# Kernel tuning notes

Hardware: AMD Instinct MI355X
Metric: run time of the kernel (lower is better)

## Reference

```python
import jax, jax.numpy as jnp
import numpy as np

D_MODEL = 1024
D_FF = 4096
FFN_H = int(2 * D_FF / 3)  # 2730, per SwiGLUMLP
B, S = 4, 4096
LN_EPS = 1e-5
ATTN_EPS = 1e-6


def layer_norm(x, g, b):
    mu = jnp.mean(x, axis=-1, keepdims=True)
    var = jnp.mean(jnp.square(x - mu), axis=-1, keepdims=True)
    return (x - mu) * jax.lax.rsqrt(var + LN_EPS) * g + b


def setup_inputs() -> dict:
    key = jax.random.key(0)
    ks = jax.random.split(key, 16)
    s = 0.02
    return {
        "x": jax.random.normal(ks[0], (B, S, D_MODEL), dtype=jnp.float32),
        "Wqkv": jax.random.normal(ks[1], (D_MODEL, 3 * D_MODEL), dtype=jnp.float32) * s,
        "bqkv": jnp.zeros((3 * D_MODEL,), jnp.float32),
        "Wg": jax.random.normal(ks[2], (D_MODEL, FFN_H), dtype=jnp.float32) * s,
        "bg": jnp.zeros((FFN_H,), jnp.float32),
        "Wu": jax.random.normal(ks[3], (D_MODEL, FFN_H), dtype=jnp.float32) * s,
        "bu": jnp.zeros((FFN_H,), jnp.float32),
        "Wd": jax.random.normal(ks[4], (FFN_H, D_MODEL), dtype=jnp.float32) * s,
        "bd": jnp.zeros((D_MODEL,), jnp.float32),
        "g1": jnp.ones((D_MODEL,), jnp.float32),
        "b1": jnp.zeros((D_MODEL,), jnp.float32),
        "g2": jnp.ones((D_MODEL,), jnp.float32),
        "b2": jnp.zeros((D_MODEL,), jnp.float32),
    }


def reference(x, Wqkv, bqkv, Wg, bg, Wu, bu, Wd, bd, g1, b1, g2, b2):
    # QKV projection, split into q, k, v (each [B,S,D])
    qkv = jnp.einsum("bsd,de->bse", x, Wqkv) + bqkv
    q, k, v = jnp.split(qkv, 3, axis=-1)

    # Linear attention with elu(x)+1 feature map (non-causal)
    qp = jax.nn.elu(q) + 1.0
    kp = jax.nn.elu(k) + 1.0
    kv = jnp.einsum("bsd,bse->bde", kp, v)        # [B,D,D] context
    num = jnp.einsum("bsd,bde->bse", qp, kv)       # [B,S,D]
    k_sum = jnp.sum(kp, axis=1)                    # [B,D]
    den = jnp.einsum("bsd,bd->bs", qp, k_sum)[..., None]
    attn = num / (den + ATTN_EPS)

    x = layer_norm(x + attn, g1, b1)

    # SwiGLU MLP
    gate = jnp.einsum("bsd,dh->bsh", x, Wg) + bg
    up = jnp.einsum("bsd,dh->bsh", x, Wu) + bu
    ffn = jnp.einsum("bsh,hd->bsd", jax.nn.silu(gate) * up, Wd) + bd

    return layer_norm(x + ffn, g2, b2)
```

## Files before the change

### kernel.cpp

```cpp
#include <hip/hip_runtime.h>

#define SEQ 4096
#define TOK 16384
#define DM 1024
#define NQKV 3072
#define FFH 2730
#define FFHP 2816

typedef __bf16 bf16x8 __attribute__((ext_vector_type(8)));
typedef float f32x4 __attribute__((ext_vector_type(4)));

__device__ __forceinline__ unsigned short f2bf(float f) {
  union { float f; unsigned u; } v; v.f = f;
  unsigned r = v.u + 0x7fffu + ((v.u >> 16) & 1u);
  return (unsigned short)(r >> 16);
}
__device__ __forceinline__ float bf2f(unsigned short h) {
  union { unsigned u; float f; } v; v.u = ((unsigned)h) << 16;
  return v.f;
}

__device__ __forceinline__ void xcd_swizzle(int& bx, int& by) {
  const int gx = gridDim.x, gy = gridDim.y;
  const int chunk = gy >> 3;
  const int csh = __ffs(chunk) - 1;
  const int lin = by * gx + bx;
  const int xcd = lin & 7, j = lin >> 3;
  by = xcd * chunk + (j & (chunk - 1));
  bx = j >> csh;
}

enum { M_QKV = 0, M_BF16 = 1, M_NUM = 2, M_BIAS_F32 = 5 };

template<int MODE>
__global__ __launch_bounds__(256)
void gemm_kernel(const unsigned short* __restrict__ A,
                 const unsigned short* __restrict__ BT,
                 int K, int lda, int ldb, int ldc,
                 long zsA, long zsB, long zsC,
                 void* __restrict__ out0, void* __restrict__ out1, void* __restrict__ out2,
                 const float* __restrict__ bias, int nbias)
{
  __shared__ unsigned short As[2][128 * 64];
  __shared__ unsigned short Bs[2][128 * 64];
  const int tid  = threadIdx.x;
  const int wave = tid >> 6, lane = tid & 63;
  const int quad = lane >> 4, l16 = lane & 15;
  const int bz = blockIdx.z;
  int bx = blockIdx.x, by = blockIdx.y;
  xcd_swizzle(bx, by);

  const unsigned short* Ab = A + (size_t)zsA * bz + (size_t)by * 128 * lda;
  const unsigned short* Bb = BT + (size_t)zsB * bz + (size_t)bx * 128 * ldb;

  f32x4 acc[4][4] = {};

  const int srow   = lane >> 3;
  const int scol_g = (((lane & 7) ^ srow) * 8);
  const int axor   = l16 & 7;

  auto stage = [&](int buf, int k0) {
#pragma unroll
    for (int j = 0; j < 4; ++j) {
      int c = wave * 4 + j;
      const unsigned short* sa = Ab + (size_t)(c * 8 + srow) * lda + k0 + scol_g;
      __builtin_amdgcn_global_load_lds((__attribute__((address_space(1))) void*)sa,
          (__attribute__((address_space(3))) void*)(As[buf] + c * 512), 16, 0, 0);
      const unsigned short* sb = Bb + (size_t)(c * 8 + srow) * ldb + k0 + scol_g;
      __builtin_amdgcn_global_load_lds((__attribute__((address_space(1))) void*)sb,
          (__attribute__((address_space(3))) void*)(Bs[buf] + c * 512), 16, 0, 0);
    }
  };

  const int NIT = K >> 6;
  stage(0, 0);
  int cur = 0;
  for (int it = 0; it < NIT; ++it) {
    __builtin_amdgcn_s_waitcnt(0);
    __syncthreads();
    if (it + 1 < NIT) stage(cur ^ 1, (it + 1) << 6);
#pragma unroll
    for (int kk = 0; kk < 64; kk += 32) {
      bf16x8 af[4], bfr[4];
#pragma unroll
      for (int mt = 0; mt < 4; ++mt)
        af[mt] = *(const bf16x8*)(As[cur] + ((wave >> 1) * 64 + mt * 16 + l16) * 64
                                     + ((((kk >> 3) + quad) ^ axor) * 8));
#pragma unroll
      for (int nt = 0; nt < 4; ++nt)
        bfr[nt] = *(const bf16x8*)(Bs[cur] + ((wave & 1) * 64 + nt * 16 + l16) * 64
                                      + ((((kk >> 3) + quad) ^ axor) * 8));
#pragma unroll
      for (int mt = 0; mt < 4; ++mt)
#pragma unroll
        for (int nt = 0; nt < 4; ++nt)
          acc[mt][nt] = __builtin_amdgcn_mfma_f32_16x16x32_bf16(af[mt], bfr[nt], acc[mt][nt], 0, 0, 0);
    }
    cur ^= 1;
  }

#pragma unroll
  for (int mt = 0; mt < 4; ++mt) {
#pragma unroll
    for (int nt = 0; nt < 4; ++nt) {
      const int r0 = by * 128 + (wave >> 1) * 64 + mt * 16 + quad * 4;
      const int c  = bx * 128 + (wave & 1) * 64 + nt * 16 + l16;
      float vals[4];
#pragma unroll
      for (int i = 0; i < 4; ++i) vals[i] = acc[mt][nt][i];

      if (MODE == M_QKV) {
        const int b = r0 >> 12, s0 = r0 & 4095;
#pragma unroll
        for (int i = 0; i < 4; ++i) vals[i] += bias[c];
        if (c < 1024) {
#pragma unroll
          for (int i = 0; i < 4; ++i) {
            float e = vals[i] > 0.f ? vals[i] + 1.f : __expf(vals[i]);
            ((unsigned short*)out0)[(size_t)(r0 + i) * DM + c] = f2bf(e);
          }
        } else if (c < 2048) {
          ushort4 o;
          float e0 = vals[0] > 0.f ? vals[0] + 1.f : __expf(vals[0]);
          float e1 = vals[1] > 0.f ? vals[1] + 1.f : __expf(vals[1]);
          float e2 = vals[2] > 0.f ? vals[2] + 1.f : __expf(vals[2]);
          float e3 = vals[3] > 0.f ? vals[3] + 1.f : __expf(vals[3]);
          o.x = f2bf(e0); o.y = f2bf(e1); o.z = f2bf(e2); o.w = f2bf(e3);
          *(ushort4*)((unsigned short*)out1 + (size_t)b * DM * SEQ + (size_t)(c - 1024) * SEQ + s0) = o;
        } else {
          ushort4 o;
          o.x = f2bf(vals[0]); o.y = f2bf(vals[1]); o.z = f2bf(vals[2]); o.w = f2bf(vals[3]);
          *(ushort4*)((unsigned short*)out2 + (size_t)b * DM * SEQ + (size_t)(c - 2048) * SEQ + s0) = o;
        }
      } else {
#pragma unroll
        for (int i = 0; i < 4; ++i) {
          const int r = r0 + i;
          float val = vals[i];
          if (MODE == M_BF16 || MODE == M_NUM) {
            ((unsigned short*)out0)[(size_t)zsC * bz + (size_t)r * ldc + c] = f2bf(val);
          } else {
            if (c < nbias) val += bias[c];
            ((float*)out0)[(size_t)r * ldc + c] = val;
          }
        }
      }
    }
  }
}

enum { G_GATEUP = 0, G_NUM = 1, G_BIAS_F32 = 2 };

#define MBAR() asm volatile("s_barrier" ::: "memory")
#define WAITV(N) asm volatile("s_waitcnt vmcnt(" #N ")" ::: "memory")

#define LDS_A(BUF, QM) do {                                                   \
    _Pragma("unroll")                                                         \
    for (int mt = 0; mt < 4; ++mt) {                                          \
      _Pragma("unroll")                                                       \
      for (int k2 = 0; k2 < 2; ++k2)                                          \
        af[mt][k2] = *(const bf16x8*)(As[BUF] +                               \
            (wm * 128 + ((QM) * 4 + mt) * 16 + l16) * 64 +                    \
            (((k2 * 4 + quad) ^ axor) * 8));                                  \
    }                                                                         \
  } while (0)

#define LDS_B(BUF, QN) do {                                                   \
    _Pragma("unroll")                                                         \
    for (int nt = 0; nt < 2; ++nt) {                                          \
      _Pragma("unroll")                                                       \
      for (int k2 = 0; k2 < 2; ++k2)                                          \
        bfr[nt][k2] = *(const bf16x8*)(Bs[BUF] +                              \
            (wn * 64 + ((QN) * 2 + nt) * 16 + l16) * 64 +                     \
            (((k2 * 4 + quad) ^ axor) * 8));                                  \
    }                                                                         \
  } while (0)

#define MMAQ(QM, QN) do {                                                     \
    _Pragma("unroll")                                                         \
    for (int mt = 0; mt < 4; ++mt) {                                          \
      _Pragma("unroll")                                                       \
      for (int nt = 0; nt < 2; ++nt) {                                        \
        _Pragma("unroll")                                                     \
        for (int k2 = 0; k2 < 2; ++k2)                                        \
          acc[(QM) * 4 + mt][(QN) * 2 + nt] =                                 \
              __builtin_amdgcn_mfma_f32_16x16x32_bf16(af[mt][k2], bfr[nt][k2],\
                  acc[(QM) * 4 + mt][(QN) * 2 + nt], 0, 0, 0);                \
      }                                                                       \
    }                                                                         \
  } while (0)

#define PHASE(BUF, QM, QN, LA, LB, STAGE, WAIT) do {                          \
    if (LA) LDS_A(BUF, QM);                                                   \
    if (LB) LDS_B(BUF, QN);                                                   \
    STAGE                                                                     \
    MBAR();                                                                   \
    __builtin_amdgcn_sched_barrier(0);                                        \
    __builtin_amdgcn_s_setprio(1);                                            \
    MMAQ(QM, QN);                                                             \
    __builtin_amdgcn_s_setprio(0);                                            \
    WAIT                                                                      \
    MBAR();                                                                   \
  } while (0)

template<int MODE>
__global__ __launch_bounds__(512, 2)
void gemm256_kernel(const unsigned short* __restrict__ A,
                    const unsigned short* __restrict__ BT,
                    int K, int lda, int ldb, int ldc,
                    long zsA, long zsB, long zsC,
                    void* __restrict__ out0,
                    const float* __restrict__ bias0,
                    const float* __restrict__ bias1,
                    int nbias)
{
  __shared__ unsigned short As[2][256 * 64];
  __shared__ unsigned short Bs[2][256 * 64];
  const int tid  = threadIdx.x;
  const int wave = tid >> 6, lane = tid & 63;
  const int quad = lane >> 4, l16 = lane & 15;
  const int wm = wave >> 2, wn = wave & 3;
  const int bz = blockIdx.z;
  int bx = blockIdx.x, by = blockIdx.y;
  xcd_swizzle(bx, by);

  const unsigned short* Ab = A + (size_t)zsA * bz + (size_t)by * 256 * lda;
  const unsigned short* Bb = BT + (size_t)zsB * bz + (size_t)bx * 256 * ldb;

  f32x4 acc[8][4] = {};

  const int srow = lane >> 3;
  const int sxor = ((lane & 7) ^ srow) * 8;
  const int axor = l16 & 7;

  const unsigned short* pA[2][2];
  const unsigned short* pB[2][2];
  int cA[2][2], cB[2][2];
#pragma unroll
  for (int part = 0; part < 2; ++part) {
#pragma unroll
    for (int j = 0; j < 2; ++j) {
      int idx = wave * 2 + j;
      int ca = ((idx & 8) ? idx + 8 : idx) + part * 8;
      int cb = (idx >> 2) * 8 + (idx & 3) + part * 4;
      cA[part][j] = ca; cB[part][j] = cb;
      pA[part][j] = Ab + (size_t)(ca * 8 + srow) * lda + sxor;
      pB[part][j] = Bb + (size_t)(cb * 8 + srow) * ldb + sxor;
    }
  }

  auto stageA = [&](int buf, int part, int tile) {
    const int k0 = tile << 6;
#pragma unroll
    for (int j = 0; j < 2; ++j)
      __builtin_amdgcn_global_load_lds(
          (__attribute__((address_space(1))) void*)(pA[part][j] + k0),
          (__attribute__((address_space(3))) void*)(As[buf] + cA[part][j] * 512), 16, 0, 0);
  };
  auto stageB = [&](int buf, int part, int tile) {
    const int k0 = tile << 6;
#pragma unroll
    for (int j = 0; j < 2; ++j)
      __builtin_amdgcn_global_load_lds(
          (__attribute__((address_space(1))) void*)(pB[part][j] + k0),
          (__attribute__((address_space(3))) void*)(Bs[buf] + cB[part][j] * 512), 16, 0, 0);
  };

  stageA(0, 0, 0); stageA(0, 1, 0); stageB(0, 0, 0); stageB(0, 1, 0);
  stageB(1, 0, 1); stageA(1, 1, 1);
  WAITV(4);
  MBAR();

  bf16x8 af[4][2], bfr[2][2];
  const int NT = K >> 6;
  for (int i = 0; i < NT; i += 2) {
    const int t1 = i + 1;
    const int t2s = (i + 2 < NT), t3s = (i + 3 < NT);
    PHASE(0, 0, 0, 1, 1, { stageA(1, 0, t1); }, {});
    PHASE(0, 1, 0, 1, 0, { stageB(1, 1, t1); }, {});
    PHASE(0, 1, 1, 0, 1, { if (t2s) stageB(0, 0, i + 2); }, {});
    PHASE(0, 0, 1, 1, 0, { if (t2s) stageA(0, 1, i + 2); },
                         { if (t2s) { WAITV(4); } else { WAITV(0); } });
    PHASE(1, 0, 0, 1, 1, { if (t2s) stageA(0, 0, i + 2); }, {});
    PHASE(1, 1, 0, 1, 0, { if (t2s) stageB(0, 1, i + 2); }, {});
    PHASE(1, 1, 1, 0, 1, { if (t3s) stageB(1, 0, i + 3); }, {});
    PHASE(1, 0, 1, 1, 0, { if (t3s) stageA(1, 1, i + 3); },
                         { if (t3s) { WAITV(4); } else { WAITV(0); } });
  }

  if (MODE == G_GATEUP) {
#pragma unroll
    for (int mt = 0; mt < 8; ++mt) {
      const int r0 = by * 256 + wm * 128 + mt * 16 + quad * 4;
#pragma unroll
      for (int p = 0; p < 2; ++p) {
        const int hc = bx * 128 + wn * 32 + p * 16 + l16;
        const float bgv = (hc < nbias) ? bias0[hc] : 0.f;
        const float buv = (hc < nbias) ? bias1[hc] : 0.f;
#pragma unroll
        for (int i2 = 0; i2 < 4; ++i2) {
          float g = acc[mt][2 * p][i2] + bgv;
          float u = acc[mt][2 * p + 1][i2] + buv;
          float hv = g / (1.f + __expf(-g)) * u;
          ((unsigned short*)out0)[(size_t)(r0 + i2) * ldc + hc] = f2bf(hv);
        }
      }
    }
  } else {
#pragma unroll
    for (int mt = 0; mt < 8; ++mt) {
#pragma unroll
      for (int nt = 0; nt < 4; ++nt) {
        const int r0 = by * 256 + wm * 128 + mt * 16 + quad * 4;
        const int c  = bx * 256 + wn * 64 + nt * 16 + l16;
#pragma unroll
        for (int i2 = 0; i2 < 4; ++i2) {
          float v = acc[mt][nt][i2];
          if (MODE == G_NUM) {
            ((unsigned short*)out0)[(size_t)zsC * bz + (size_t)(r0 + i2) * ldc + c] = f2bf(v);
          } else {
            if (c < nbias) v += bias0[c];
            ((float*)out0)[(size_t)(r0 + i2) * ldc + c] = v;
          }
        }
      }
    }
  }
}

__global__ __launch_bounds__(256)
void cvt_kernel(const float* __restrict__ in, unsigned short* __restrict__ out, int n)
{
  int i = (blockIdx.x * 256 + threadIdx.x) * 4;
  if (i < n) {
    float4 v = *(const float4*)(in + i);
    ushort4 o;
    o.x = f2bf(v.x); o.y = f2bf(v.y); o.z = f2bf(v.z); o.w = f2bf(v.w);
    *(ushort4*)(out + i) = o;
  }
}

__global__ __launch_bounds__(256)
void wtrans_kernel(const float* __restrict__ in, unsigned short* __restrict__ out,
                   int R, int C, int Cpad, int Rpad, int omode)
{
  __shared__ float tile[32][33];
  int r0 = blockIdx.x * 32;
  int c0 = blockIdx.y * 32;
  int tid = threadIdx.x;
#pragma unroll
  for (int j = 0; j < 4; ++j) {
    int r = j * 8 + (tid >> 5), c = tid & 31;
    float v = 0.f;
    if (r0 + r < R && c0 + c < C) v = in[(size_t)(r0 + r) * C + c0 + c];
    tile[r][c] = v;
  }
  __syncthreads();
#pragma unroll
  for (int j = 0; j < 4; ++j) {
    int c = j * 8 + (tid >> 5), r = tid & 31;
    int oc = c0 + c;
    int orow = (omode == 0) ? oc
             : ((oc >> 4) * 32 + (oc & 15) + ((omode == 2) ? 16 : 0));
    out[(size_t)orow * Rpad + (r0 + r)] = f2bf(tile[r][c]);
  }
}

__device__ __forceinline__ float block_sum(float v, float* sm)
{
#pragma unroll
  for (int o = 32; o > 0; o >>= 1) v += __shfl_down(v, o, 64);
  int w = threadIdx.x >> 6;
  if ((threadIdx.x & 63) == 0) sm[w] = v;
  __syncthreads();
  float r = sm[0] + sm[1] + sm[2] + sm[3];
  __syncthreads();
  return r;
}

__global__ __launch_bounds__(256)
void ksum_kernel(const unsigned short* __restrict__ kpT, float* __restrict__ ksum)
{
  __shared__ float sm[4];
  int row = blockIdx.x;
  const ushort4* src = (const ushort4*)(kpT + (size_t)row * SEQ);
  float s = 0.f;
#pragma unroll
  for (int j = 0; j < 4; ++j) {
    ushort4 v = src[threadIdx.x + j * 256];
    s += bf2f(v.x) + bf2f(v.y) + bf2f(v.z) + bf2f(v.w);
  }
  float tot = block_sum(s, sm);
  if (threadIdx.x == 0) ksum[row] = tot;
}

__global__ __launch_bounds__(256)
void ln1_kernel(const unsigned short* __restrict__ xb16, const unsigned short* __restrict__ num16,
                const unsigned short* __restrict__ qp, const float* __restrict__ ksum,
                const float* __restrict__ g1, const float* __restrict__ b1,
                unsigned short* __restrict__ yb)
{
  __shared__ float sm[4];
  int t = blockIdx.x, tid = threadIdx.x, b = t >> 12;
  ushort4 xv = ((const ushort4*)(xb16 + (size_t)t * DM))[tid];
  ushort4 nv = ((const ushort4*)(num16 + (size_t)t * DM))[tid];
  ushort4 qv = ((const ushort4*)(qp + (size_t)t * DM))[tid];
  float4 kv = ((const float4*)(ksum + (size_t)b * DM))[tid];
  float q0 = bf2f(qv.x), q1 = bf2f(qv.y), q2 = bf2f(qv.z), q3 = bf2f(qv.w);
  float den = block_sum(q0 * kv.x + q1 * kv.y + q2 * kv.z + q3 * kv.w, sm);
  float inv = 1.f / (den + 1e-6f);
  float r0 = bf2f(xv.x) + bf2f(nv.x) * inv, r1 = bf2f(xv.y) + bf2f(nv.y) * inv;
  float r2 = bf2f(xv.z) + bf2f(nv.z) * inv, r3 = bf2f(xv.w) + bf2f(nv.w) * inv;
  float s1 = block_sum(r0 + r1 + r2 + r3, sm);
  float s2 = block_sum(r0 * r0 + r1 * r1 + r2 * r2 + r3 * r3, sm);
  float mu = s1 * (1.f / 1024.f);
  float var = s2 * (1.f / 1024.f) - mu * mu;
  float rs = rsqrtf(var + 1e-5f);
  float4 gv = ((const float4*)g1)[tid];
  float4 bv = ((const float4*)b1)[tid];
  ushort4 o;
  o.x = f2bf((r0 - mu) * rs * gv.x + bv.x);
  o.y = f2bf((r1 - mu) * rs * gv.y + bv.y);
  o.z = f2bf((r2 - mu) * rs * gv.z + bv.z);
  o.w = f2bf((r3 - mu) * rs * gv.w + bv.w);
  ((ushort4*)(yb + (size_t)t * DM))[tid] = o;
}

__global__ __launch_bounds__(256)
void ln2_kernel(const unsigned short* __restrict__ yb, const float* __restrict__ ffn,
                const float* __restrict__ g2, const float* __restrict__ b2,
                float* __restrict__ out)
{
  __shared__ float sm[4];
  int t = blockIdx.x, tid = threadIdx.x;
  ushort4 yv = ((const ushort4*)(yb + (size_t)t * DM))[tid];
  float4 fv = ((const float4*)(ffn + (size_t)t * DM))[tid];
  float r0 = bf2f(yv.x) + fv.x, r1 = bf2f(yv.y) + fv.y;
  float r2 = bf2f(yv.z) + fv.z, r3 = bf2f(yv.w) + fv.w;
  float s1 = block_sum(r0 + r1 + r2 + r3, sm);
  float s2 = block_sum(r0 * r0 + r1 * r1 + r2 * r2 + r3 * r3, sm);
  float mu = s1 * (1.f / 1024.f);
  float var = s2 * (1.f / 1024.f) - mu * mu;
  float rs = rsqrtf(var + 1e-5f);
  float4 gv = ((const float4*)g2)[tid];
  float4 bv = ((const float4*)b2)[tid];
  float4 o;
  o.x = (r0 - mu) * rs * gv.x + bv.x;
  o.y = (r1 - mu) * rs * gv.y + bv.y;
  o.z = (r2 - mu) * rs * gv.z + bv.z;
  o.w = (r3 - mu) * rs * gv.w + bv.w;
  ((float4*)(out + (size_t)t * DM))[tid] = o;
}

extern "C" void kernel_launch(void* const* d_in, const int* in_sizes, int n_in,
                              void* d_out, int out_size, void* d_ws, size_t ws_size,
                              hipStream_t stream)
{
  const float* x    = (const float*)d_in[0];
  const float* Wqkv = (const float*)d_in[1];
  const float* bqkv = (const float*)d_in[2];
  const float* Wg   = (const float*)d_in[3];
  const float* bg   = (const float*)d_in[4];
  const float* Wu   = (const float*)d_in[5];
  const float* bu   = (const float*)d_in[6];
  const float* Wd   = (const float*)d_in[7];
  const float* bd   = (const float*)d_in[8];
  const float* g1   = (const float*)d_in[9];
  const float* b1   = (const float*)d_in[10];
  const float* g2   = (const float*)d_in[11];
  const float* b2   = (const float*)d_in[12];
  float* out = (float*)d_out;

  char* ws = (char*)d_ws;
  size_t off = 0;
  auto alloc = [&](size_t bytes) {
    char* p = ws + off;
    off += (bytes + 255) & ~(size_t)255;
    return p;
  };
  unsigned short* WqkvT = (unsigned short*)alloc((size_t)NQKV * DM * 2);
  unsigned short* WguT  = (unsigned short*)alloc((size_t)2 * FFHP * DM * 2);
  unsigned short* WdT   = (unsigned short*)alloc((size_t)DM * FFHP * 2);
  float*          ksum  = (float*)alloc((size_t)4 * DM * 4);
  unsigned short* xbyb  = (unsigned short*)alloc((size_t)TOK * DM * 2);
  unsigned short* kvT   = (unsigned short*)alloc((size_t)4 * DM * DM * 2);
  char* R3 = alloc((size_t)3 * TOK * DM * 2);
  unsigned short* qp  = (unsigned short*)(R3);
  unsigned short* kpT = (unsigned short*)(R3 + (size_t)TOK * DM * 2);
  unsigned short* vT  = (unsigned short*)(R3 + (size_t)2 * TOK * DM * 2);
  unsigned short* hbuf = (unsigned short*)(R3);
  unsigned short* xb = xbyb;
  unsigned short* yb = xbyb;
  unsigned short* num = (unsigned short*)d_out;
  float* ffn = (float*)d_out;

  dim3 blk(256), blk5(512);

  cvt_kernel<<<dim3(TOK * DM / 1024), blk, 0, stream>>>(x, xb, TOK * DM);
  wtrans_kernel<<<dim3(32, 96), blk, 0, stream>>>(Wqkv, WqkvT, 1024, 3072, 3072, 1024, 0);
  wtrans_kernel<<<dim3(32, 88), blk, 0, stream>>>(Wg, WguT, 1024, FFH, FFHP, 1024, 1);
  wtrans_kernel<<<dim3(32, 88), blk, 0, stream>>>(Wu, WguT, 1024, FFH, FFHP, 1024, 2);
  wtrans_kernel<<<dim3(88, 32), blk, 0, stream>>>(Wd, WdT, FFH, 1024, 1024, FFHP, 0);
  gemm_kernel<M_QKV><<<dim3(NQKV / 128, TOK / 128), blk, 0, stream>>>(
      xb, WqkvT, 1024, 1024, 1024, 0, 0, 0, 0, qp, kpT, vT, bqkv, NQKV);
  ksum_kernel<<<dim3(4096), blk, 0, stream>>>(kpT, ksum);
  gemm_kernel<M_BF16><<<dim3(8, 8, 4), blk, 0, stream>>>(
      vT, kpT, 4096, 4096, 4096, 1024,
      (long)DM * SEQ, (long)DM * SEQ, (long)DM * DM,
      kvT, nullptr, nullptr, nullptr, 0);
  gemm256_kernel<G_NUM><<<dim3(4, 16, 4), blk5, 0, stream>>>(
      qp, kvT, 1024, 1024, 1024, 1024,
      (long)SEQ * DM, (long)DM * DM, (long)SEQ * DM,
      num, nullptr, nullptr, 0);
  ln1_kernel<<<dim3(TOK), blk, 0, stream>>>(xb, num, qp, ksum, g1, b1, yb);
  gemm256_kernel<G_GATEUP><<<dim3(2 * FFHP / 256, TOK / 256), blk5, 0, stream>>>(
      yb, WguT, 1024, DM, DM, FFHP, 0, 0, 0, hbuf, bg, bu, FFH);
  gemm256_kernel<G_BIAS_F32><<<dim3(DM / 256, TOK / 256), blk5, 0, stream>>>(
      hbuf, WdT, FFHP, FFHP, FFHP, DM, 0, 0, 0, ffn, bd, nullptr, DM);
  ln2_kernel<<<dim3(TOK), blk, 0, stream>>>(yb, ffn, g2, b2, out);

  (void)in_sizes; (void)n_in; (void)out_size; (void)ws_size;
}
```

Before: 787.7 us.

## Move QKV projection onto 256x256 pipelined GEMM with LDS-transposed K/V epilogue

New measurement: 741.2 us. -5.9%, faster.

```diff
diff --git a/kernel.cpp b/kernel.cpp
--- a/kernel.cpp
+++ b/kernel.cpp
@@ -9,6 +9,7 @@
 
 typedef __bf16 bf16x8 __attribute__((ext_vector_type(8)));
 typedef float f32x4 __attribute__((ext_vector_type(4)));
+typedef unsigned short u16x8 __attribute__((ext_vector_type(8)));
 
 __device__ __forceinline__ unsigned short f2bf(float f) {
   union { float f; unsigned u; } v; v.f = f;
@@ -105,51 +106,22 @@
     for (int nt = 0; nt < 4; ++nt) {
       const int r0 = by * 128 + (wave >> 1) * 64 + mt * 16 + quad * 4;
       const int c  = bx * 128 + (wave & 1) * 64 + nt * 16 + l16;
-      float vals[4];
-#pragma unroll
-      for (int i = 0; i < 4; ++i) vals[i] = acc[mt][nt][i];
-
-      if (MODE == M_QKV) {
-        const int b = r0 >> 12, s0 = r0 & 4095;
-#pragma unroll
-        for (int i = 0; i < 4; ++i) vals[i] += bias[c];
-        if (c < 1024) {
-#pragma unroll
-          for (int i = 0; i < 4; ++i) {
-            float e = vals[i] > 0.f ? vals[i] + 1.f : __expf(vals[i]);
-            ((unsigned short*)out0)[(size_t)(r0 + i) * DM + c] = f2bf(e);
-          }
-        } else if (c < 2048) {
-          ushort4 o;
-          float e0 = vals[0] > 0.f ? vals[0] + 1.f : __expf(vals[0]);
-          float e1 = vals[1] > 0.f ? vals[1] + 1.f : __expf(vals[1]);
-          float e2 = vals[2] > 0.f ? vals[2] + 1.f : __expf(vals[2]);
-          float e3 = vals[3] > 0.f ? vals[3] + 1.f : __expf(vals[3]);
-          o.x = f2bf(e0); o.y = f2bf(e1); o.z = f2bf(e2); o.w = f2bf(e3);
-          *(ushort4*)((unsigned short*)out1 + (size_t)b * DM * SEQ + (size_t)(c - 1024) * SEQ + s0) = o;
+#pragma unroll
+      for (int i = 0; i < 4; ++i) {
+        const int r = r0 + i;
+        float val = acc[mt][nt][i];
+        if (MODE == M_BF16 || MODE == M_NUM) {
+          ((unsigned short*)out0)[(size_t)zsC * bz + (size_t)r * ldc + c] = f2bf(val);
         } else {
-          ushort4 o;
-          o.x = f2bf(vals[0]); o.y = f2bf(vals[1]); o.z = f2bf(vals[2]); o.w = f2bf(vals[3]);
-          *(ushort4*)((unsigned short*)out2 + (size_t)b * DM * SEQ + (size_t)(c - 2048) * SEQ + s0) = o;
-        }
-      } else {
-#pragma unroll
-        for (int i = 0; i < 4; ++i) {
-          const int r = r0 + i;
-          float val = vals[i];
-          if (MODE == M_BF16 || MODE == M_NUM) {
-            ((unsigned short*)out0)[(size_t)zsC * bz + (size_t)r * ldc + c] = f2bf(val);
-          } else {
-            if (c < nbias) val += bias[c];
-            ((float*)out0)[(size_t)r * ldc + c] = val;
-          }
+          if (c < nbias) val += bias[c];
+          ((float*)out0)[(size_t)r * ldc + c] = val;
         }
       }
     }
   }
 }
 
-enum { G_GATEUP = 0, G_NUM = 1, G_BIAS_F32 = 2 };
+enum { G_GATEUP = 0, G_NUM = 1, G_BIAS_F32 = 2, G_QKV = 3 };
 
 #define MBAR() asm volatile("s_barrier" ::: "memory")
 #define WAITV(N) asm volatile("s_waitcnt vmcnt(" #N ")" ::: "memory")
@@ -159,7 +131,7 @@
     for (int mt = 0; mt < 4; ++mt) {                                          \
       _Pragma("unroll")                                                       \
       for (int k2 = 0; k2 < 2; ++k2)                                          \
-        af[mt][k2] = *(const bf16x8*)(As[BUF] +                               \
+        af[mt][k2] = *(const bf16x8*)(SH[BUF] +                               \
             (wm * 128 + ((QM) * 4 + mt) * 16 + l16) * 64 +                    \
             (((k2 * 4 + quad) ^ axor) * 8));                                  \
     }                                                                         \
@@ -170,7 +142,7 @@
     for (int nt = 0; nt < 2; ++nt) {                                          \
       _Pragma("unroll")                                                       \
       for (int k2 = 0; k2 < 2; ++k2)                                          \
-        bfr[nt][k2] = *(const bf16x8*)(Bs[BUF] +                              \
+        bfr[nt][k2] = *(const bf16x8*)(SH[2 + (BUF)] +                        \
             (wn * 64 + ((QN) * 2 + nt) * 16 + l16) * 64 +                     \
             (((k2 * 4 + quad) ^ axor) * 8));                                  \
     }                                                                         \
@@ -210,12 +182,12 @@
                     int K, int lda, int ldb, int ldc,
                     long zsA, long zsB, long zsC,
                     void* __restrict__ out0,
+                    void* __restrict__ out1, void* __restrict__ out2,
                     const float* __restrict__ bias0,
                     const float* __restrict__ bias1,
                     int nbias)
 {
-  __shared__ unsigned short As[2][256 * 64];
-  __shared__ unsigned short Bs[2][256 * 64];
+  __shared__ unsigned short SH[4][256 * 64];
   const int tid  = threadIdx.x;
   const int wave = tid >> 6, lane = tid & 63;
   const int quad = lane >> 4, l16 = lane & 15;
@@ -255,7 +227,7 @@
     for (int j = 0; j < 2; ++j)
       __builtin_amdgcn_global_load_lds(
           (__attribute__((address_space(1))) void*)(pA[part][j] + k0),
-          (__attribute__((address_space(3))) void*)(As[buf] + cA[part][j] * 512), 16, 0, 0);
+          (__attribute__((address_space(3))) void*)(SH[buf] + cA[part][j] * 512), 16, 0, 0);
   };
   auto stageB = [&](int buf, int part, int tile) {
     const int k0 = tile << 6;
@@ -263,29 +235,28 @@
     for (int j = 0; j < 2; ++j)
       __builtin_amdgcn_global_load_lds(
           (__attribute__((address_space(1))) void*)(pB[part][j] + k0),
-          (__attribute__((address_space(3))) void*)(Bs[buf] + cB[part][j] * 512), 16, 0, 0);
+          (__attribute__((address_space(3))) void*)(SH[2 + buf] + cB[part][j] * 512), 16, 0, 0);
   };
 
-  stageA(0, 0, 0); stageA(0, 1, 0); stageB(0, 0, 0); stageB(0, 1, 0);
-  stageB(1, 0, 1); stageA(1, 1, 1);
+  stageA(0, 0, 0); stageB(0, 0, 0); stageA(0, 1, 0); stageB(0, 1, 0);
+  stageA(1, 0, 1); stageA(1, 1, 1);
   WAITV(4);
   MBAR();
 
   bf16x8 af[4][2], bfr[2][2];
   const int NT = K >> 6;
   for (int i = 0; i < NT; i += 2) {
-    const int t1 = i + 1;
-    const int t2s = (i + 2 < NT), t3s = (i + 3 < NT);
-    PHASE(0, 0, 0, 1, 1, { stageA(1, 0, t1); }, {});
-    PHASE(0, 1, 0, 1, 0, { stageB(1, 1, t1); }, {});
-    PHASE(0, 1, 1, 0, 1, { if (t2s) stageB(0, 0, i + 2); }, {});
-    PHASE(0, 0, 1, 1, 0, { if (t2s) stageA(0, 1, i + 2); },
+    const int t2s = (i + 2 < NT);
+    PHASE(0, 0, 0, 1, 1, { stageB(1, 0, i + 1); }, {});
+    PHASE(0, 0, 1, 0, 1, { stageB(1, 1, i + 1); }, {});
+    PHASE(0, 1, 1, 1, 0, { if (t2s) stageA(0, 0, i + 2); }, {});
+    PHASE(0, 1, 0, 0, 1, { if (t2s) stageB(0, 1, i + 2); },
                          { if (t2s) { WAITV(4); } else { WAITV(0); } });
-    PHASE(1, 0, 0, 1, 1, { if (t2s) stageA(0, 0, i + 2); }, {});
-    PHASE(1, 1, 0, 1, 0, { if (t2s) stageB(0, 1, i + 2); }, {});
-    PHASE(1, 1, 1, 0, 1, { if (t3s) stageB(1, 0, i + 3); }, {});
-    PHASE(1, 0, 1, 1, 0, { if (t3s) stageA(1, 1, i + 3); },
-                         { if (t3s) { WAITV(4); } else { WAITV(0); } });
+    PHASE(1, 0, 0, 1, 1, { if (t2s) stageA(0, 1, i + 2); }, {});
+    PHASE(1, 0, 1, 0, 1, { if (t2s) stageB(0, 0, i + 2); }, {});
+    PHASE(1, 1, 1, 1, 0, { if (t2s) stageA(1, 0, i + 3); }, {});
+    PHASE(1, 1, 0, 0, 1, { if (t2s) stageA(1, 1, i + 3); },
+                         { if (t2s) { WAITV(4); } else { WAITV(0); } });
   }
 
   if (MODE == G_GATEUP) {
@@ -304,6 +275,55 @@
           float hv = g / (1.f + __expf(-g)) * u;
           ((unsigned short*)out0)[(size_t)(r0 + i2) * ldc + hc] = f2bf(hv);
         }
+      }
+    }
+  } else if (MODE == G_QKV) {
+    const int b = (by * 256) >> 12, s0 = (by * 256) & 4095;
+    if (bx < 4) {
+#pragma unroll
+      for (int mt = 0; mt < 8; ++mt) {
+#pragma unroll
+        for (int nt = 0; nt < 4; ++nt) {
+          const int r0 = by * 256 + wm * 128 + mt * 16 + quad * 4;
+          const int c  = bx * 256 + wn * 64 + nt * 16 + l16;
+          const float bv = bias0[c];
+#pragma unroll
+          for (int i2 = 0; i2 < 4; ++i2) {
+            float v = acc[mt][nt][i2] + bv;
+            float e = v > 0.f ? v + 1.f : __expf(v);
+            ((unsigned short*)out0)[(size_t)(r0 + i2) * DM + c] = f2bf(e);
+          }
+        }
+      }
+    } else {
+      const bool isK = (bx < 8);
+      unsigned short* lsc = &SH[0][0];
+#pragma unroll
+      for (int mt = 0; mt < 8; ++mt) {
+        const int sb = wm * 128 + mt * 16 + quad * 4;
+#pragma unroll
+        for (int nt = 0; nt < 4; ++nt) {
+          const int cl = wn * 64 + nt * 16 + l16;
+          const float bv = bias0[bx * 256 + cl];
+          ushort4 o;
+#pragma unroll
+          for (int i2 = 0; i2 < 4; ++i2) {
+            float v = acc[mt][nt][i2] + bv;
+            if (isK) v = v > 0.f ? v + 1.f : __expf(v);
+            ((unsigned short*)&o)[i2] = f2bf(v);
+          }
+          *(ushort4*)(lsc + cl * 256 + (((sb >> 3) ^ (cl & 31)) << 3) + (sb & 7)) = o;
+        }
+      }
+      __syncthreads();
+      unsigned short* obase = isK ? (unsigned short*)out1 : (unsigned short*)out2;
+      const int coff = (isK ? (bx - 4) : (bx - 8)) * 256;
+      const int l32 = tid & 31;
+#pragma unroll
+      for (int pass = 0; pass < 16; ++pass) {
+        const int c = pass * 16 + (tid >> 5);
+        u16x8 v = *(const u16x8*)(lsc + c * 256 + ((l32 ^ (c & 31)) << 3));
+        *(u16x8*)(obase + ((size_t)b * DM + coff + c) * SEQ + s0 + l32 * 8) = v;
       }
     }
   } else {
@@ -501,8 +521,8 @@
   wtrans_kernel<<<dim3(32, 88), blk, 0, stream>>>(Wg, WguT, 1024, FFH, FFHP, 1024, 1);
   wtrans_kernel<<<dim3(32, 88), blk, 0, stream>>>(Wu, WguT, 1024, FFH, FFHP, 1024, 2);
   wtrans_kernel<<<dim3(88, 32), blk, 0, stream>>>(Wd, WdT, FFH, 1024, 1024, FFHP, 0);
-  gemm_kernel<M_QKV><<<dim3(NQKV / 128, TOK / 128), blk, 0, stream>>>(
-      xb, WqkvT, 1024, 1024, 1024, 0, 0, 0, 0, qp, kpT, vT, bqkv, NQKV);
+  gemm256_kernel<G_QKV><<<dim3(NQKV / 256, TOK / 256), blk5, 0, stream>>>(
+      xb, WqkvT, 1024, 1024, 1024, 0, 0, 0, 0, qp, kpT, vT, bqkv, nullptr, NQKV);
   ksum_kernel<<<dim3(4096), blk, 0, stream>>>(kpT, ksum);
   gemm_kernel<M_BF16><<<dim3(8, 8, 4), blk, 0, stream>>>(
       vT, kpT, 4096, 4096, 4096, 1024,
@@ -511,12 +531,12 @@
   gemm256_kernel<G_NUM><<<dim3(4, 16, 4), blk5, 0, stream>>>(
       qp, kvT, 1024, 1024, 1024, 1024,
       (long)SEQ * DM, (long)DM * DM, (long)SEQ * DM,
-      num, nullptr, nullptr, 0);
+      num, nullptr, nullptr, nullptr, nullptr, 0);
   ln1_kernel<<<dim3(TOK), blk, 0, stream>>>(xb, num, qp, ksum, g1, b1, yb);
   gemm256_kernel<G_GATEUP><<<dim3(2 * FFHP / 256, TOK / 256), blk5, 0, stream>>>(
-      yb, WguT, 1024, DM, DM, FFHP, 0, 0, 0, hbuf, bg, bu, FFH);
+      yb, WguT, 1024, DM, DM, FFHP, 0, 0, 0, hbuf, nullptr, nullptr, bg, bu, FFH);
   gemm256_kernel<G_BIAS_F32><<<dim3(DM / 256, TOK / 256), blk5, 0, stream>>>(
-      hbuf, WdT, FFHP, FFHP, FFHP, DM, 0, 0, 0, ffn, bd, nullptr, DM);
+      hbuf, WdT, FFHP, FFHP, FFHP, DM, 0, 0, 0, ffn, nullptr, nullptr, bd, nullptr, DM);
   ln2_kernel<<<dim3(TOK), blk, 0, stream>>>(yb, ffn, g2, b2, out);
 
   (void)in_sizes; (void)n_in; (void)out_size; (void)ws_size;
```
